# Performance work log

Hardware: AMD Instinct MI355X
Metric: run time of the kernel (lower is better)

## Reference

```python
import jax, jax.numpy as jnp
import numpy as np

N = 50000          # nodes
E = 1600000        # edges (avg degree 32)
F_IN = 1280        # ESM node feature dim
H = 128            # hidden (128x0e irreps)
G = 64             # graphs in batch
OUT = 2
SH0 = 0.5 / np.sqrt(np.pi)   # Y_00 under e3nn 'integral' normalization (constant; l=1,2 sh
                             # have zero CG coupling into 0e outputs, so only l=0 survives)
TP_NORM = SH0 / np.sqrt(H)   # path weight normalization 1/sqrt(fan_in), fan_in = mul_in1*mul_in2 = H*1


def _mean_aggregate(msg, dst, num_nodes):
    # scatter-mean of per-edge messages onto destination nodes (PyG aggr='mean')
    s = jax.ops.segment_sum(msg, dst, num_segments=num_nodes)
    cnt = jax.ops.segment_sum(jnp.ones((msg.shape[0],), msg.dtype), dst, num_segments=num_nodes)
    return s / jnp.maximum(cnt, 1.0)[:, None]


def _equivariant_conv(h, edge_index, tp_w):
    # EquivariantConv: gather x_j, tensor product with sh(edge_vec), scatter-mean.
    # edge_vec normalization is irrelevant for the surviving l=0 path (Y_00 is constant).
    src, dst = edge_index[0], edge_index[1]
    msg = (h[src] @ tp_w) * TP_NORM            # [E, H]
    return _mean_aggregate(msg, dst, h.shape[0])


def setup_inputs() -> dict:
    key = jax.random.key(0)
    ks = jax.random.split(key, 16)
    inp = {
        "x": jax.random.normal(ks[0], (N, F_IN), jnp.float32),
        "pos": jax.random.normal(ks[1], (N, 3), jnp.float32),
        "edge_index": jax.random.randint(ks[2], (2, E), 0, N),
        "batch": jnp.sort(jax.random.randint(ks[3], (N,), 0, G)),
        # lin_in (xavier-like scale)
        "lin_w": jax.random.normal(ks[4], (F_IN, H), jnp.float32) * (1.0 / np.sqrt(F_IN)),
        "lin_b": jnp.zeros((H,), jnp.float32),
        # FullyConnectedTensorProduct internal weights ~ N(0,1), shape [mul_in, mul_out]
        "tp_w1": jax.random.normal(ks[5], (H, H), jnp.float32),
        "tp_w2": jax.random.normal(ks[6], (H, H), jnp.float32),
        "tp_w3": jax.random.normal(ks[7], (H, H), jnp.float32),
        # classifier
        "c1w": jax.random.normal(ks[8], (H, H), jnp.float32) * (1.0 / np.sqrt(H)),
        "c1b": jnp.zeros((H,), jnp.float32),
        "c2w": jax.random.normal(ks[9], (H, H), jnp.float32) * (1.0 / np.sqrt(H)),
        "c2b": jnp.zeros((H,), jnp.float32),
        "c3w": jax.random.normal(ks[10], (H, OUT), jnp.float32) * (1.0 / np.sqrt(H)),
        "c3b": jnp.zeros((OUT,), jnp.float32),
    }
    return inp


def reference(x, pos, edge_index, batch, lin_w, lin_b, tp_w1, tp_w2, tp_w3,
              c1w, c1b, c2w, c2b, c3w, c3b):
    h = jax.nn.relu(x @ lin_w + lin_b)                    # lin_in + relu (dropout p=0, eval)
    h = jax.nn.relu(_equivariant_conv(h, edge_index, tp_w1))
    h = jax.nn.relu(_equivariant_conv(h, edge_index, tp_w2))
    h = _equivariant_conv(h, edge_index, tp_w3)           # no relu after conv3
    # global_mean_pool over graphs
    s = jax.ops.segment_sum(h, batch, num_segments=G)
    cnt = jax.ops.segment_sum(jnp.ones((h.shape[0],), h.dtype), batch, num_segments=G)
    z = s / jnp.maximum(cnt, 1.0)[:, None]                # [G, H]
    o = jax.nn.relu(z @ c1w + c1b)
    o = jax.nn.relu(o @ c2w + c2b)
    out = o @ c3w + c3b                                   # [G, OUT]
    return (out, z)
```

## Files before the change

kernel.cpp:

```cpp
#include <hip/hip_runtime.h>
#include <hip/hip_bf16.h>

typedef __bf16 bf16_t;
typedef bf16_t bf16x4 __attribute__((ext_vector_type(4)));
typedef bf16_t bf16x8 __attribute__((ext_vector_type(8)));
typedef float f32x4 __attribute__((ext_vector_type(4)));

static constexpr int N_NODES = 50000;
static constexpr int N_EDGES = 1600000;
static constexpr int FIN = 1280;
static constexpr int HD = 128;
static constexpr int NG = 64;
static constexpr float TP_NORM_F = 0.0249338908f;

__global__ __launch_bounds__(256) void k_transpose_scale(const float* __restrict__ src,
                                                         bf16_t* __restrict__ dst,
                                                         int K, float scale) {
  int idx = blockIdx.x * 256 + threadIdx.x;
  if (idx >= K * HD) return;
  int k = idx >> 7, n = idx & 127;
  dst[n * K + k] = (bf16_t)(src[idx] * scale);
}

template <typename AT>
__global__ __launch_bounds__(256) void k_gemm32(const AT* __restrict__ A,
                                                const bf16_t* __restrict__ Bt,
                                                const float* __restrict__ bias,
                                                bf16_t* __restrict__ C,
                                                int M, int K, int doRelu) {
  __shared__ bf16_t As[32 * 64];
  __shared__ bf16_t Bs[128 * 64];
  const int t = threadIdx.x;
  const int wid = t >> 6;
  const int lane = t & 63;
  const int wn = wid * 32;
  const int l15 = lane & 15;
  const int quad = lane >> 4;
  const int rowBase = blockIdx.x * 32;

  f32x4 acc[2][2];
#pragma unroll
  for (int i = 0; i < 2; ++i)
#pragma unroll
    for (int j = 0; j < 2; ++j) {
      f32x4 z = {0.f, 0.f, 0.f, 0.f};
      acc[i][j] = z;
    }

  for (int k0 = 0; k0 < K; k0 += 64) {
    if constexpr (sizeof(AT) == 4) {
#pragma unroll
      for (int i = 0; i < 2; ++i) {
        int idx = t + i * 256;
        int row = idx >> 4;
        int col4 = idx & 15;
        int gr = rowBase + row;
        float4 v = make_float4(0.f, 0.f, 0.f, 0.f);
        if (gr < M) v = *(const float4*)(A + (size_t)gr * K + k0 + col4 * 4);
        bf16x4 w;
        w[0] = (bf16_t)v.x; w[1] = (bf16_t)v.y; w[2] = (bf16_t)v.z; w[3] = (bf16_t)v.w;
        int c = col4 >> 1;
        int off = row * 64 + ((c ^ (row & 7)) << 3) + ((col4 & 1) << 2);
        *(bf16x4*)&As[off] = w;
      }
    } else {
      int row = t >> 3;
      int c = t & 7;
      int gr = rowBase + row;
      bf16x8 v = {};
      if (gr < M) v = *(const bf16x8*)(A + (size_t)gr * K + k0 + c * 8);
      int off = row * 64 + ((c ^ (row & 7)) << 3);
      *(bf16x8*)&As[off] = v;
    }
#pragma unroll
    for (int i = 0; i < 4; ++i) {
      int idx = t + i * 256;
      int row = idx >> 3;
      int c = idx & 7;
      bf16x8 v = *(const bf16x8*)(Bt + (size_t)row * K + k0 + c * 8);
      int off = row * 64 + ((c ^ (row & 7)) << 3);
      *(bf16x8*)&Bs[off] = v;
    }
    __syncthreads();
#pragma unroll
    for (int kk = 0; kk < 2; ++kk) {
      bf16x8 af[2], bfr[2];
      int k8 = kk * 4 + quad;
#pragma unroll
      for (int mi = 0; mi < 2; ++mi) {
        int row = mi * 16 + l15;
        af[mi] = *(const bf16x8*)&As[row * 64 + ((k8 ^ (row & 7)) << 3)];
      }
#pragma unroll
      for (int ni = 0; ni < 2; ++ni) {
        int row = wn + ni * 16 + l15;
        bfr[ni] = *(const bf16x8*)&Bs[row * 64 + ((k8 ^ (row & 7)) << 3)];
      }
#pragma unroll
      for (int mi = 0; mi < 2; ++mi)
#pragma unroll
        for (int ni = 0; ni < 2; ++ni)
          acc[mi][ni] = __builtin_amdgcn_mfma_f32_16x16x32_bf16(af[mi], bfr[ni], acc[mi][ni], 0, 0, 0);
    }
    __syncthreads();
  }

#pragma unroll
  for (int mi = 0; mi < 2; ++mi) {
#pragma unroll
    for (int ni = 0; ni < 2; ++ni) {
      int col = wn + ni * 16 + l15;
      float bv = bias ? bias[col] : 0.f;
#pragma unroll
      for (int r = 0; r < 4; ++r) {
        int row = mi * 16 + quad * 4 + r;
        int gr = rowBase + row;
        if (gr < M) {
          float v = acc[mi][ni][r] + bv;
          if (doRelu) v = fmaxf(v, 0.f);
          C[(size_t)gr * HD + col] = (bf16_t)v;
        }
      }
    }
  }
}

__global__ __launch_bounds__(256) void k_pos(const int* __restrict__ dst, int* __restrict__ cnt,
                                             int* __restrict__ pos, int E) {
  int e = blockIdx.x * 256 + threadIdx.x;
  if (e < E) pos[e] = atomicAdd(&cnt[dst[e]], 1);
}

__global__ __launch_bounds__(256) void k_scan1(const int* __restrict__ cnt, int* __restrict__ bsum, int n) {
  __shared__ int s[256];
  int t = threadIdx.x;
  int i = blockIdx.x * 256 + t;
  s[t] = (i < n) ? cnt[i] : 0;
  __syncthreads();
  for (int d = 128; d > 0; d >>= 1) {
    if (t < d) s[t] += s[t + d];
    __syncthreads();
  }
  if (t == 0) bsum[blockIdx.x] = s[0];
}

__global__ __launch_bounds__(256) void k_scan2(int* __restrict__ bsum, int nb) {
  __shared__ int s[256];
  int t = threadIdx.x;
  int v = (t < nb) ? bsum[t] : 0;
  s[t] = v;
  __syncthreads();
  for (int d = 1; d < 256; d <<= 1) {
    int x = (t >= d) ? s[t - d] : 0;
    __syncthreads();
    s[t] += x;
    __syncthreads();
  }
  if (t < nb) bsum[t] = s[t] - v;
  if (t == 255) bsum[nb] = s[255];
}

__global__ __launch_bounds__(256) void k_scan3(const int* __restrict__ cnt, const int* __restrict__ bsum,
                                               int* __restrict__ off, int n) {
  __shared__ int s[256];
  int t = threadIdx.x;
  int i = blockIdx.x * 256 + t;
  int v = (i < n) ? cnt[i] : 0;
  s[t] = v;
  __syncthreads();
  for (int d = 1; d < 256; d <<= 1) {
    int x = (t >= d) ? s[t - d] : 0;
    __syncthreads();
    s[t] += x;
    __syncthreads();
  }
  if (i < n) off[i] = bsum[blockIdx.x] + s[t] - v;
  if (i == n - 1) off[n] = bsum[blockIdx.x] + s[t];
}

__global__ __launch_bounds__(256) void k_fill(const int* __restrict__ src, const int* __restrict__ dst,
                                              const int* __restrict__ off, const int* __restrict__ pos,
                                              int* __restrict__ ssrc, int E) {
  int e = blockIdx.x * 256 + threadIdx.x;
  if (e >= E) return;
  ssrc[off[dst[e]] + pos[e]] = src[e];
}

__global__ __launch_bounds__(256) void k_aggregate(const bf16_t* __restrict__ h,
                                                   const int* __restrict__ ssrc,
                                                   const int* __restrict__ off,
                                                   bf16_t* __restrict__ agg, int n) {
  int node = blockIdx.x * 4 + (threadIdx.x >> 6);
  if (node >= n) return;
  int lane = threadIdx.x & 63;
  int g = lane >> 4;
  int fl = lane & 15;
  int b = off[node], e = off[node + 1];
  float acc[8];
#pragma unroll
  for (int j = 0; j < 8; ++j) acc[j] = 0.f;
  const bf16_t* hp = h + fl * 8;
  int i = b;
  for (; i + 8 <= e; i += 8) {
    int s0 = ssrc[i + g];
    int s1 = ssrc[i + 4 + g];
    bf16x8 v0 = *(const bf16x8*)(hp + (size_t)s0 * HD);
    bf16x8 v1 = *(const bf16x8*)(hp + (size_t)s1 * HD);
#pragma unroll
    for (int j = 0; j < 8; ++j) acc[j] += (float)v0[j] + (float)v1[j];
  }
  if (i + 4 <= e) {
    int s0 = ssrc[i + g];
    bf16x8 v0 = *(const bf16x8*)(hp + (size_t)s0 * HD);
#pragma unroll
    for (int j = 0; j < 8; ++j) acc[j] += (float)v0[j];
    i += 4;
  }
  if (i + g < e) {
    int s0 = ssrc[i + g];
    bf16x8 v0 = *(const bf16x8*)(hp + (size_t)s0 * HD);
#pragma unroll
    for (int j = 0; j < 8; ++j) acc[j] += (float)v0[j];
  }
#pragma unroll
  for (int j = 0; j < 8; ++j) {
    acc[j] += __shfl_xor(acc[j], 16);
    acc[j] += __shfl_xor(acc[j], 32);
  }
  if (g == 0) {
    float inv = (e > b) ? 1.f / (float)(e - b) : 0.f;
    bf16x8 o;
#pragma unroll
    for (int j = 0; j < 8; ++j) o[j] = (bf16_t)(acc[j] * inv);
    *(bf16x8*)(agg + (size_t)node * HD + fl * 8) = o;
  }
}

__global__ __launch_bounds__(128) void k_pool(const bf16_t* __restrict__ agg, const int* __restrict__ batch,
                                              float* __restrict__ p, float* __restrict__ gcnt, int n) {
  int base = blockIdx.x * 256;
  if (base >= n) return;
  int t = threadIdx.x;
  int end = min(base + 256, n);
  float acc = 0.f;
  int curg = batch[base];
  int runStart = base;
  for (int i = base; i < end; ++i) {
    int g = batch[i];
    if (g != curg) {
      atomicAdd(&p[curg * HD + t], acc);
      if (t == 0) atomicAdd(&gcnt[curg], (float)(i - runStart));
      acc = 0.f; curg = g; runStart = i;
    }
    acc += (float)agg[(size_t)i * HD + t];
  }
  atomicAdd(&p[curg * HD + t], acc);
  if (t == 0) atomicAdd(&gcnt[curg], (float)(end - runStart));
}

__global__ __launch_bounds__(128) void k_head(const float* __restrict__ p, const float* __restrict__ gcnt,
                                              const float* __restrict__ w3,
                                              const float* __restrict__ c1w, const float* __restrict__ c1b,
                                              const float* __restrict__ c2w, const float* __restrict__ c2b,
                                              const float* __restrict__ c3w, const float* __restrict__ c3b,
                                              float* __restrict__ out) {
  __shared__ float sa[128], sb[128];
  int g = blockIdx.x, t = threadIdx.x;
  float inv = 1.f / fmaxf(gcnt[g], 1.f);
  sa[t] = p[g * HD + t] * inv;
  __syncthreads();
  float z = 0.f;
  for (int k = 0; k < HD; ++k) z += sa[k] * w3[k * HD + t];
  z *= TP_NORM_F;
  out[128 + g * HD + t] = z;
  sb[t] = z;
  __syncthreads();
  float o1 = c1b[t];
  for (int k = 0; k < HD; ++k) o1 += sb[k] * c1w[k * HD + t];
  o1 = fmaxf(o1, 0.f);
  __syncthreads();
  sa[t] = o1;
  __syncthreads();
  float o2 = c2b[t];
  for (int k = 0; k < HD; ++k) o2 += sa[k] * c2w[k * HD + t];
  o2 = fmaxf(o2, 0.f);
  __syncthreads();
  sb[t] = o2;
  __syncthreads();
  if (t < 2) {
    float o = c3b[t];
    for (int k = 0; k < HD; ++k) o += sb[k] * c3w[k * 2 + t];
    out[g * 2 + t] = o;
  }
}

extern "C" void kernel_launch(void* const* d_in, const int* in_sizes, int n_in,
                              void* d_out, int out_size, void* d_ws, size_t ws_size,
                              hipStream_t stream) {
  const float* x = (const float*)d_in[0];
  const int* eidx = (const int*)d_in[2];
  const int* src = eidx;
  const int* dst = eidx + N_EDGES;
  const int* batch = (const int*)d_in[3];
  const float* lin_w = (const float*)d_in[4];
  const float* lin_b = (const float*)d_in[5];
  const float* tp_w1 = (const float*)d_in[6];
  const float* tp_w2 = (const float*)d_in[7];
  const float* tp_w3 = (const float*)d_in[8];
  const float* c1w = (const float*)d_in[9];
  const float* c1b = (const float*)d_in[10];
  const float* c2w = (const float*)d_in[11];
  const float* c2b = (const float*)d_in[12];
  const float* c3w = (const float*)d_in[13];
  const float* c3b = (const float*)d_in[14];
  float* out = (float*)d_out;
  (void)in_sizes; (void)n_in; (void)out_size; (void)ws_size;

  uintptr_t wp = (uintptr_t)d_ws;
  auto alloc = [&](size_t bytes) -> void* {
    uintptr_t a = (wp + 255) & ~(uintptr_t)255;
    wp = a + bytes;
    return (void*)a;
  };
  bf16_t* WtL  = (bf16_t*)alloc(sizeof(bf16_t) * (size_t)HD * FIN);
  bf16_t* Wt1  = (bf16_t*)alloc(sizeof(bf16_t) * (size_t)HD * HD);
  bf16_t* Wt2  = (bf16_t*)alloc(sizeof(bf16_t) * (size_t)HD * HD);
  bf16_t* h    = (bf16_t*)alloc(sizeof(bf16_t) * (size_t)50048 * HD);
  bf16_t* agg  = (bf16_t*)alloc(sizeof(bf16_t) * (size_t)50048 * HD);
  int*    cnt  = (int*)alloc(sizeof(int) * N_NODES);
  int*    bsum = (int*)alloc(sizeof(int) * 256);
  int*    offs = (int*)alloc(sizeof(int) * (N_NODES + 1));
  int*    pos  = (int*)alloc(sizeof(int) * N_EDGES);
  int*    ssrc = (int*)alloc(sizeof(int) * N_EDGES);
  float*  pbuf = (float*)alloc(sizeof(float) * NG * HD);
  float*  gcnt = (float*)alloc(sizeof(float) * NG);

  hipMemsetAsync(cnt, 0, sizeof(int) * N_NODES, stream);
  hipMemsetAsync(pbuf, 0, sizeof(float) * NG * HD, stream);
  hipMemsetAsync(gcnt, 0, sizeof(float) * NG, stream);

  k_transpose_scale<<<(FIN * HD + 255) / 256, 256, 0, stream>>>(lin_w, WtL, FIN, 1.0f);
  k_transpose_scale<<<(HD * HD + 255) / 256, 256, 0, stream>>>(tp_w1, Wt1, HD, TP_NORM_F);
  k_transpose_scale<<<(HD * HD + 255) / 256, 256, 0, stream>>>(tp_w2, Wt2, HD, TP_NORM_F);

  const int nScanBlocks = (N_NODES + 255) / 256;
  k_pos<<<(N_EDGES + 255) / 256, 256, 0, stream>>>(dst, cnt, pos, N_EDGES);
  k_scan1<<<nScanBlocks, 256, 0, stream>>>(cnt, bsum, N_NODES);
  k_scan2<<<1, 256, 0, stream>>>(bsum, nScanBlocks);
  k_scan3<<<nScanBlocks, 256, 0, stream>>>(cnt, bsum, offs, N_NODES);
  k_fill<<<(N_EDGES + 255) / 256, 256, 0, stream>>>(src, dst, offs, pos, ssrc, N_EDGES);

  const int gblocks = (N_NODES + 31) / 32;
  const int ablocks = (N_NODES + 3) / 4;

  k_gemm32<float><<<gblocks, 256, 0, stream>>>(x, WtL, lin_b, h, N_NODES, FIN, 1);

  k_aggregate<<<ablocks, 256, 0, stream>>>(h, ssrc, offs, agg, N_NODES);
  k_gemm32<bf16_t><<<gblocks, 256, 0, stream>>>(agg, Wt1, nullptr, h, N_NODES, HD, 1);
  k_aggregate<<<ablocks, 256, 0, stream>>>(h, ssrc, offs, agg, N_NODES);
  k_gemm32<bf16_t><<<gblocks, 256, 0, stream>>>(agg, Wt2, nullptr, h, N_NODES, HD, 1);
  k_aggregate<<<ablocks, 256, 0, stream>>>(h, ssrc, offs, agg, N_NODES);

  k_pool<<<(N_NODES + 255) / 256, 128, 0, stream>>>(agg, batch, pbuf, gcnt, N_NODES);
  k_head<<<NG, 128, 0, stream>>>(pbuf, gcnt, tp_w3, c1w, c1b, c2w, c2b, c3w, c3b, out);
}
```

Baseline: 782.2 us.

## Replace LDS-tiled GEMM with per-wave streaming MFMA, restructure pool and transposes

The shared-memory tiled GEMM is replaced by a kernel where each wavefront computes 16 rows by all 128 columns. It streams A directly from global memory and reads B fragments from global or cache with no LDS and no barriers. Separately, the three weight transposes are merged into one launch, and the aggregate loop is unrolled to 16 edges to get more loads in flight. Pooling now uses one block per graph with a binary search over the sorted batch vector, which removes the atomics and memsets. The risks are more global or L2 traffic for B without LDS reuse, and the GEMM assumes N is a multiple of 16 because there is no row bound check.

```diff
diff --git a/kernel.cpp b/kernel.cpp
--- a/kernel.cpp
+++ b/kernel.cpp
@@ -13,114 +13,81 @@
 static constexpr int NG = 64;
 static constexpr float TP_NORM_F = 0.0249338908f;
 
-__global__ __launch_bounds__(256) void k_transpose_scale(const float* __restrict__ src,
-                                                         bf16_t* __restrict__ dst,
-                                                         int K, float scale) {
+__global__ __launch_bounds__(256) void k_transpose_all(const float* __restrict__ lin_w,
+                                                       const float* __restrict__ tp_w1,
+                                                       const float* __restrict__ tp_w2,
+                                                       bf16_t* __restrict__ WtL,
+                                                       bf16_t* __restrict__ Wt1,
+                                                       bf16_t* __restrict__ Wt2) {
   int idx = blockIdx.x * 256 + threadIdx.x;
-  if (idx >= K * HD) return;
-  int k = idx >> 7, n = idx & 127;
-  dst[n * K + k] = (bf16_t)(src[idx] * scale);
+  const int A1 = FIN * HD;
+  const int A2 = A1 + HD * HD;
+  const int A3 = A2 + HD * HD;
+  if (idx < A1) {
+    int k = idx >> 7, n = idx & 127;
+    WtL[n * FIN + k] = (bf16_t)lin_w[idx];
+  } else if (idx < A2) {
+    int j = idx - A1;
+    int k = j >> 7, n = j & 127;
+    Wt1[n * HD + k] = (bf16_t)(tp_w1[j] * TP_NORM_F);
+  } else if (idx < A3) {
+    int j = idx - A2;
+    int k = j >> 7, n = j & 127;
+    Wt2[n * HD + k] = (bf16_t)(tp_w2[j] * TP_NORM_F);
+  }
 }
 
 template <typename AT>
-__global__ __launch_bounds__(256) void k_gemm32(const AT* __restrict__ A,
-                                                const bf16_t* __restrict__ Bt,
-                                                const float* __restrict__ bias,
-                                                bf16_t* __restrict__ C,
-                                                int M, int K, int doRelu) {
-  __shared__ bf16_t As[32 * 64];
-  __shared__ bf16_t Bs[128 * 64];
-  const int t = threadIdx.x;
-  const int wid = t >> 6;
-  const int lane = t & 63;
-  const int wn = wid * 32;
+__global__ __launch_bounds__(256) void k_gemm_stream(const AT* __restrict__ A,
+                                                     const bf16_t* __restrict__ Bt,
+                                                     const float* __restrict__ bias,
+                                                     bf16_t* __restrict__ C,
+                                                     int M, int K, int doRelu) {
+  const int w = (blockIdx.x * 256 + threadIdx.x) >> 6;
+  if (w * 16 >= M) return;
+  const int lane = threadIdx.x & 63;
   const int l15 = lane & 15;
   const int quad = lane >> 4;
-  const int rowBase = blockIdx.x * 32;
-
-  f32x4 acc[2][2];
-#pragma unroll
-  for (int i = 0; i < 2; ++i)
-#pragma unroll
-    for (int j = 0; j < 2; ++j) {
-      f32x4 z = {0.f, 0.f, 0.f, 0.f};
-      acc[i][j] = z;
+  const int rowA = w * 16 + l15;
+
+  f32x4 acc[8];
+#pragma unroll
+  for (int t = 0; t < 8; ++t) {
+    f32x4 z = {0.f, 0.f, 0.f, 0.f};
+    acc[t] = z;
+  }
+
+  const AT* ap = A + (size_t)rowA * K + quad * 8;
+  const bf16_t* bp = Bt + (size_t)l15 * K + quad * 8;
+
+#pragma unroll 2
+  for (int k0 = 0; k0 < K; k0 += 32) {
+    bf16x8 af;
+    if constexpr (sizeof(AT) == 4) {
+      f32x4 a0 = *(const f32x4*)(ap + k0);
+      f32x4 a1 = *(const f32x4*)(ap + k0 + 4);
+#pragma unroll
+      for (int j = 0; j < 4; ++j) { af[j] = (bf16_t)a0[j]; af[j + 4] = (bf16_t)a1[j]; }
+    } else {
+      af = *(const bf16x8*)(ap + k0);
     }
-
-  for (int k0 = 0; k0 < K; k0 += 64) {
-    if constexpr (sizeof(AT) == 4) {
-#pragma unroll
-      for (int i = 0; i < 2; ++i) {
-        int idx = t + i * 256;
-        int row = idx >> 4;
-        int col4 = idx & 15;
-        int gr = rowBase + row;
-        float4 v = make_float4(0.f, 0.f, 0.f, 0.f);
-        if (gr < M) v = *(const float4*)(A + (size_t)gr * K + k0 + col4 * 4);
-        bf16x4 w;
-        w[0] = (bf16_t)v.x; w[1] = (bf16_t)v.y; w[2] = (bf16_t)v.z; w[3] = (bf16_t)v.w;
-        int c = col4 >> 1;
-        int off = row * 64 + ((c ^ (row & 7)) << 3) + ((col4 & 1) << 2);
-        *(bf16x4*)&As[off] = w;
-      }
-    } else {
-      int row = t >> 3;
-      int c = t & 7;
-      int gr = rowBase + row;
-      bf16x8 v = {};
-      if (gr < M) v = *(const bf16x8*)(A + (size_t)gr * K + k0 + c * 8);
-      int off = row * 64 + ((c ^ (row & 7)) << 3);
-      *(bf16x8*)&As[off] = v;
+#pragma unroll
+    for (int t = 0; t < 8; ++t) {
+      bf16x8 bf = *(const bf16x8*)(bp + (size_t)t * 16 * K + k0);
+      acc[t] = __builtin_amdgcn_mfma_f32_16x16x32_bf16(af, bf, acc[t], 0, 0, 0);
     }
-#pragma unroll
-    for (int i = 0; i < 4; ++i) {
-      int idx = t + i * 256;
-      int row = idx >> 3;
-      int c = idx & 7;
-      bf16x8 v = *(const bf16x8*)(Bt + (size_t)row * K + k0 + c * 8);
-      int off = row * 64 + ((c ^ (row & 7)) << 3);
-      *(bf16x8*)&Bs[off] = v;
-    }
-    __syncthreads();
-#pragma unroll
-    for (int kk = 0; kk < 2; ++kk) {
-      bf16x8 af[2], bfr[2];
-      int k8 = kk * 4 + quad;
-#pragma unroll
-      for (int mi = 0; mi < 2; ++mi) {
-        int row = mi * 16 + l15;
-        af[mi] = *(const bf16x8*)&As[row * 64 + ((k8 ^ (row & 7)) << 3)];
-      }
-#pragma unroll
-      for (int ni = 0; ni < 2; ++ni) {
-        int row = wn + ni * 16 + l15;
-        bfr[ni] = *(const bf16x8*)&Bs[row * 64 + ((k8 ^ (row & 7)) << 3)];
-      }
-#pragma unroll
-      for (int mi = 0; mi < 2; ++mi)
-#pragma unroll
-        for (int ni = 0; ni < 2; ++ni)
-          acc[mi][ni] = __builtin_amdgcn_mfma_f32_16x16x32_bf16(af[mi], bfr[ni], acc[mi][ni], 0, 0, 0);
-    }
-    __syncthreads();
-  }
-
-#pragma unroll
-  for (int mi = 0; mi < 2; ++mi) {
-#pragma unroll
-    for (int ni = 0; ni < 2; ++ni) {
-      int col = wn + ni * 16 + l15;
-      float bv = bias ? bias[col] : 0.f;
-#pragma unroll
-      for (int r = 0; r < 4; ++r) {
-        int row = mi * 16 + quad * 4 + r;
-        int gr = rowBase + row;
-        if (gr < M) {
-          float v = acc[mi][ni][r] + bv;
-          if (doRelu) v = fmaxf(v, 0.f);
-          C[(size_t)gr * HD + col] = (bf16_t)v;
-        }
-      }
+  }
+
+#pragma unroll
+  for (int t = 0; t < 8; ++t) {
+    int col = t * 16 + l15;
+    float bv = bias ? bias[col] : 0.f;
+#pragma unroll
+    for (int r = 0; r < 4; ++r) {
+      int gr = w * 16 + quad * 4 + r;
+      float v = acc[t][r] + bv;
+      if (doRelu) v = fmaxf(v, 0.f);
+      C[(size_t)gr * HD + col] = (bf16_t)v;
     }
   }
 }
@@ -201,13 +168,27 @@
   for (int j = 0; j < 8; ++j) acc[j] = 0.f;
   const bf16_t* hp = h + fl * 8;
   int i = b;
-  for (; i + 8 <= e; i += 8) {
+  for (; i + 16 <= e; i += 16) {
+    int s0 = ssrc[i + g];
+    int s1 = ssrc[i + 4 + g];
+    int s2 = ssrc[i + 8 + g];
+    int s3 = ssrc[i + 12 + g];
+    bf16x8 v0 = *(const bf16x8*)(hp + (size_t)s0 * HD);
+    bf16x8 v1 = *(const bf16x8*)(hp + (size_t)s1 * HD);
+    bf16x8 v2 = *(const bf16x8*)(hp + (size_t)s2 * HD);
+    bf16x8 v3 = *(const bf16x8*)(hp + (size_t)s3 * HD);
+#pragma unroll
+    for (int j = 0; j < 8; ++j)
+      acc[j] += ((float)v0[j] + (float)v1[j]) + ((float)v2[j] + (float)v3[j]);
+  }
+  if (i + 8 <= e) {
     int s0 = ssrc[i + g];
     int s1 = ssrc[i + 4 + g];
     bf16x8 v0 = *(const bf16x8*)(hp + (size_t)s0 * HD);
     bf16x8 v1 = *(const bf16x8*)(hp + (size_t)s1 * HD);
 #pragma unroll
     for (int j = 0; j < 8; ++j) acc[j] += (float)v0[j] + (float)v1[j];
+    i += 8;
   }
   if (i + 4 <= e) {
     int s0 = ssrc[i + g];
@@ -236,29 +217,32 @@
   }
 }
 
-__global__ __launch_bounds__(128) void k_pool(const bf16_t* __restrict__ agg, const int* __restrict__ batch,
-                                              float* __restrict__ p, float* __restrict__ gcnt, int n) {
-  int base = blockIdx.x * 256;
-  if (base >= n) return;
+__global__ __launch_bounds__(256) void k_pool(const bf16_t* __restrict__ agg,
+                                              const int* __restrict__ batch,
+                                              float* __restrict__ p, int n) {
+  __shared__ float s[256];
+  int g = blockIdx.x;
   int t = threadIdx.x;
-  int end = min(base + 256, n);
+  int lo = 0, hi = n;
+  while (lo < hi) { int m = (lo + hi) >> 1; if (batch[m] < g) lo = m + 1; else hi = m; }
+  int lo2 = lo, hi2 = n;
+  while (lo2 < hi2) { int m = (lo2 + hi2) >> 1; if (batch[m] < g + 1) lo2 = m + 1; else hi2 = m; }
+  int count = lo2 - lo;
+  int f = t & 127;
+  int half = t >> 7;
   float acc = 0.f;
-  int curg = batch[base];
-  int runStart = base;
-  for (int i = base; i < end; ++i) {
-    int g = batch[i];
-    if (g != curg) {
-      atomicAdd(&p[curg * HD + t], acc);
-      if (t == 0) atomicAdd(&gcnt[curg], (float)(i - runStart));
-      acc = 0.f; curg = g; runStart = i;
-    }
-    acc += (float)agg[(size_t)i * HD + t];
-  }
-  atomicAdd(&p[curg * HD + t], acc);
-  if (t == 0) atomicAdd(&gcnt[curg], (float)(end - runStart));
-}
-
-__global__ __launch_bounds__(128) void k_head(const float* __restrict__ p, const float* __restrict__ gcnt,
+  for (int i = lo + half; i < lo2; i += 2)
+    acc += (float)agg[(size_t)i * HD + f];
+  s[t] = acc;
+  __syncthreads();
+  if (t < 128) {
+    float v = s[t] + s[t + 128];
+    float inv = (count > 0) ? 1.f / (float)count : 0.f;
+    p[g * HD + t] = v * inv;
+  }
+}
+
+__global__ __launch_bounds__(128) void k_head(const float* __restrict__ p,
                                               const float* __restrict__ w3,
                                               const float* __restrict__ c1w, const float* __restrict__ c1b,
                                               const float* __restrict__ c2w, const float* __restrict__ c2b,
@@ -266,8 +250,7 @@
                                               float* __restrict__ out) {
   __shared__ float sa[128], sb[128];
   int g = blockIdx.x, t = threadIdx.x;
-  float inv = 1.f / fmaxf(gcnt[g], 1.f);
-  sa[t] = p[g * HD + t] * inv;
+  sa[t] = p[g * HD + t];
   __syncthreads();
   float z = 0.f;
   for (int k = 0; k < HD; ++k) z += sa[k] * w3[k * HD + t];
@@ -333,15 +316,11 @@
   int*    pos  = (int*)alloc(sizeof(int) * N_EDGES);
   int*    ssrc = (int*)alloc(sizeof(int) * N_EDGES);
   float*  pbuf = (float*)alloc(sizeof(float) * NG * HD);
-  float*  gcnt = (float*)alloc(sizeof(float) * NG);
 
   hipMemsetAsync(cnt, 0, sizeof(int) * N_NODES, stream);
-  hipMemsetAsync(pbuf, 0, sizeof(float) * NG * HD, stream);
-  hipMemsetAsync(gcnt, 0, sizeof(float) * NG, stream);
-
-  k_transpose_scale<<<(FIN * HD + 255) / 256, 256, 0, stream>>>(lin_w, WtL, FIN, 1.0f);
-  k_transpose_scale<<<(HD * HD + 255) / 256, 256, 0, stream>>>(tp_w1, Wt1, HD, TP_NORM_F);
-  k_transpose_scale<<<(HD * HD + 255) / 256, 256, 0, stream>>>(tp_w2, Wt2, HD, TP_NORM_F);
+
+  k_transpose_all<<<(FIN * HD + 2 * HD * HD + 255) / 256, 256, 0, stream>>>(
+      lin_w, tp_w1, tp_w2, WtL, Wt1, Wt2);
 
   const int nScanBlocks = (N_NODES + 255) / 256;
   k_pos<<<(N_EDGES + 255) / 256, 256, 0, stream>>>(dst, cnt, pos, N_EDGES);
@@ -350,17 +329,18 @@
   k_scan3<<<nScanBlocks, 256, 0, stream>>>(cnt, bsum, offs, N_NODES);
   k_fill<<<(N_EDGES + 255) / 256, 256, 0, stream>>>(src, dst, offs, pos, ssrc, N_EDGES);
 
-  const int gblocks = (N_NODES + 31) / 32;
+  const int nWaves = N_NODES / 16;
+  const int gblocks = (nWaves + 3) / 4;
   const int ablocks = (N_NODES + 3) / 4;
 
-  k_gemm32<float><<<gblocks, 256, 0, stream>>>(x, WtL, lin_b, h, N_NODES, FIN, 1);
+  k_gemm_stream<float><<<gblocks, 256, 0, stream>>>(x, WtL, lin_b, h, N_NODES, FIN, 1);
 
   k_aggregate<<<ablocks, 256, 0, stream>>>(h, ssrc, offs, agg, N_NODES);
-  k_gemm32<bf16_t><<<gblocks, 256, 0, stream>>>(agg, Wt1, nullptr, h, N_NODES, HD, 1);
+  k_gemm_stream<bf16_t><<<gblocks, 256, 0, stream>>>(agg, Wt1, nullptr, h, N_NODES, HD, 1);
   k_aggregate<<<ablocks, 256, 0, stream>>>(h, ssrc, offs, agg, N_NODES);
-  k_gemm32<bf16_t><<<gblocks, 256, 0, stream>>>(agg, Wt2, nullptr, h, N_NODES, HD, 1);
+  k_gemm_stream<bf16_t><<<gblocks, 256, 0, stream>>>(agg, Wt2, nullptr, h, N_NODES, HD, 1);
   k_aggregate<<<ablocks, 256, 0, stream>>>(h, ssrc, offs, agg, N_NODES);
 
-  k_pool<<<(N_NODES + 255) / 256, 128, 0, stream>>>(agg, batch, pbuf, gcnt, N_NODES);
-  k_head<<<NG, 128, 0, stream>>>(pbuf, gcnt, tp_w3, c1w, c1b, c2w, c2b, c3w, c3b, out);
-}
+  k_pool<<<NG, 256, 0, stream>>>(agg, batch, pbuf, N_NODES);
+  k_head<<<NG, 128, 0, stream>>>(pbuf, tp_w3, c1w, c1b, c2w, c2b, c3w, c3b, out);
+}
```

After: 914.6 us. 1.17x slower.
